# Kernel tuning notes

Hardware: AMD Instinct MI355X
Metric: run time of the kernel (lower is better)

Reference implementation:

```python
import jax, jax.numpy as jnp
import numpy as np

EPS = 1e-6  # matches nn.CosineSimilarity(eps=1e-6) and the log-denominator eps


def setup_inputs() -> dict:
    key = jax.random.key(0)
    k1, k2 = jax.random.split(key)
    bs, d = 8192, 128
    f = jax.random.normal(k1, (bs, d), dtype=jnp.float32)
    noise = jax.random.normal(k2, (bs, d), dtype=jnp.float32)
    return {"f": f, "noise": noise}


def reference(f, noise):
    bs = f.shape[0]
    cat = jnp.concatenate([noise, f], axis=0)  # [2bs, d]
    # torch CosineSimilarity: x.y / max(||x||*||y||, eps)
    nf = jnp.linalg.norm(f, axis=1)    # [bs]
    nc = jnp.linalg.norm(cat, axis=1)  # [2bs]
    sims = (f @ cat.T) / jnp.maximum(nf[:, None] * nc[None, :], EPS)  # [bs, 2bs]
    m = jnp.exp(sims)
    idx = jnp.arange(bs)
    pos = m[idx, idx]                 # f[i] vs noise[i]
    self_sim = m[idx, idx + bs]       # f[i] vs f[i], excluded from negatives
    neg_sum = m.sum(axis=1) - pos - self_sim
    loss = -jnp.log(pos / (neg_sum + EPS))
    return loss.mean()
```

## Files before the change

### kernel.cpp

```cpp
#include <hip/hip_runtime.h>
#include <hip/hip_bf16.h>
#include <math.h>

#define BS 8192
#define D 128
#define NROWS 16384
#define COLS_PER_BLOCK 512
#define NCHUNK (COLS_PER_BLOCK / 16)
#define NSPLIT (NROWS / COLS_PER_BLOCK)
#define NPART NSPLIT

typedef int i32x8 __attribute__((ext_vector_type(8)));
typedef float f32x4 __attribute__((ext_vector_type(4)));

#define LN2F 0.6931471805599453f
#define STORE_SCALE 19.217958569050494f
#define E8M0_M4 123

#if __has_builtin(__builtin_amdgcn_exp2f)
#define EXP2F(x) __builtin_amdgcn_exp2f(x)
#else
#define EXP2F(x) exp2f(x)
#endif


__global__ __launch_bounds__(256) void nrm_cvt(const float* __restrict__ f,
                                               const float* __restrict__ noise,
                                               char* __restrict__ catF) {
  const int lane = threadIdx.x & 63;
  const int wv = threadIdx.x >> 6;
  const int row = blockIdx.x * 4 + wv;
  const float* src = (row < BS) ? (noise + (size_t)row * D) : (f + (size_t)(row - BS) * D);
  float2 v = ((const float2*)src)[lane];
  float ss = v.x * v.x + v.y * v.y;
#pragma unroll
  for (int m = 1; m <= 32; m <<= 1) ss += __shfl_xor(ss, m, 64);
  const float s = STORE_SCALE / sqrtf(ss);
  const int packed = __builtin_amdgcn_cvt_pk_fp8_f32(v.x * s, v.y * s, 0, false);
  char* dst = catF + ((size_t)(row >> 4) << 11) + ((lane >> 4) << 9) +
              ((row & 15) << 5) + ((lane & 15) << 1);
  *(unsigned short*)dst = (unsigned short)(packed & 0xffff);
}

__global__ __launch_bounds__(256) void infonce_main(
    const char* __restrict__ catF,
    float* __restrict__ ws_neg, float* __restrict__ ws_pos) {
  const int tid = threadIdx.x;
  const int lane = tid & 63;
  const int w = tid >> 6;
  const int l15 = lane & 15, l4 = lane >> 4;
  const int nb = blockIdx.x, mb = blockIdx.y;
  const int growbase = mb * 128 + w * 32;
  const int col0 = nb * COLS_PER_BLOCK;
  const int lbase = l4 * 512 + l15 * 32;

  i32x8 a[2];
  {
    const char* ab = catF + ((size_t)((BS + growbase) >> 4) << 11) + lbase;
    a[0] = *(const i32x8*)(ab);
    a[1] = *(const i32x8*)(ab + 2048);
  }

  f32x4 rs[2];
  const f32x4 z = {0.f, 0.f, 0.f, 0.f};
  rs[0] = z;
  rs[1] = z;

  const char* bl = catF + ((size_t)(col0 >> 4) << 11) + lbase;

  i32x8 bb[2];
  bb[0] = *(const i32x8*)(bl);

#pragma unroll
  for (int ch = 0; ch < NCHUNK; ++ch) {
    const int cu = ch & 1;
    if (ch + 1 < NCHUNK)
      bb[cu ^ 1] = *(const i32x8*)(bl + (size_t)(ch + 1) * 2048);

    f32x4 acc[2];
#pragma unroll
    for (int rf = 0; rf < 2; rf++)
      acc[rf] = __builtin_amdgcn_mfma_scale_f32_16x16x128_f8f6f4(
          a[rf], bb[cu], z, 0 , 0 ,
          0, E8M0_M4, 0, E8M0_M4);

    const int c0 = col0 + ch * 16;
    const bool dPos = (c0 >= growbase) && (c0 < growbase + 32);
    const bool dSelf = (c0 - BS >= growbase) && (c0 - BS < growbase + 32);
    if (!dPos && !dSelf) {
#pragma unroll
      for (int rf = 0; rf < 2; rf++) {
        f32x4 e;
#pragma unroll
        for (int r = 0; r < 4; r++) e[r] = EXP2F(acc[rf][r]);
        rs[rf] += e;
      }
    } else {
#pragma unroll
      for (int rf = 0; rf < 2; rf++)
#pragma unroll
        for (int r = 0; r < 4; r++) {
          const int grow = growbase + rf * 16 + l4 * 4 + r;
          const int gcol = c0 + l15;
          const float v = acc[rf][r];
          const bool ex = dPos ? (gcol == grow) : (gcol == grow + BS);
          if (dPos && gcol == grow) ws_pos[grow] = v;
          rs[rf][r] += ex ? 0.f : EXP2F(v);
        }
    }
  }

  float rowsum[8];
#pragma unroll
  for (int rf = 0; rf < 2; rf++)
#pragma unroll
    for (int r = 0; r < 4; r++) {
      float v = rs[rf][r];
      v += __shfl_xor(v, 1, 64);
      v += __shfl_xor(v, 2, 64);
      v += __shfl_xor(v, 4, 64);
      v += __shfl_xor(v, 8, 64);
      rowsum[rf * 4 + r] = v;
    }
  if (l15 == 0) {
    float* dst = ws_neg + (size_t)nb * BS + growbase;
#pragma unroll
    for (int rf = 0; rf < 2; rf++)
#pragma unroll
      for (int r = 0; r < 4; r++) dst[rf * 16 + l4 * 4 + r] = rowsum[rf * 4 + r];
  }
}

__global__ __launch_bounds__(256) void finalize1(const float* __restrict__ ws_neg,
                                                 const float* __restrict__ ws_pos,
                                                 float* __restrict__ partial) {
  const int row = blockIdx.x * 256 + threadIdx.x;
  float neg = 0.f;
#pragma unroll
  for (int p = 0; p < NPART; p++) neg += ws_neg[(size_t)p * BS + row];
  float local = logf(neg + 1e-6f) - ws_pos[row] * LN2F;
#pragma unroll
  for (int m = 1; m <= 32; m <<= 1) local += __shfl_xor(local, m, 64);
  __shared__ float red[4];
  if ((threadIdx.x & 63) == 0) red[threadIdx.x >> 6] = local;
  __syncthreads();
  if (threadIdx.x == 0) partial[blockIdx.x] = red[0] + red[1] + red[2] + red[3];
}

__global__ void finalize2(const float* __restrict__ partial, float* __restrict__ out) {
  float v = ((int)threadIdx.x < 32) ? partial[threadIdx.x] : 0.f;
#pragma unroll
  for (int m = 1; m <= 32; m <<= 1) v += __shfl_xor(v, m, 64);
  if (threadIdx.x == 0) out[0] = v * (1.f / BS);
}

extern "C" void kernel_launch(void* const* d_in, const int* in_sizes, int n_in,
                              void* d_out, int out_size, void* d_ws, size_t ws_size,
                              hipStream_t stream) {
  const float* f = (const float*)d_in[0];
  const float* noise = (const float*)d_in[1];
  char* ws = (char*)d_ws;
  char* catF = ws;
  float* ws_pos = (float*)(ws + (size_t)NROWS * D);
  float* ws_neg = ws_pos + BS;
  float* partial = ws_neg + (size_t)NPART * BS;

  nrm_cvt<<<NROWS / 4, 256, 0, stream>>>(f, noise, catF);
  dim3 grid(NSPLIT, BS / 128);
  infonce_main<<<grid, 256, 0, stream>>>(catF, ws_neg, ws_pos);
  finalize1<<<BS / 256, 256, 0, stream>>>(ws_neg, ws_pos, partial);
  finalize2<<<1, 64, 0, stream>>>(partial, (float*)d_out);
}
```

Before: 41.42 us.

## Fuse finalize into main kernel via last-block atomic, deepen B prefetch

Drops the two finalize kernel launches by having the last block to finish (tracked by an atomic counter reset in the conversion kernel) perform the row reduction and log-mean in one block. Doubles the columns per block (1024, 16 splits) and switches to a 4-deep B-fragment ring with two chunks of MFMAs issued per phase before their epilogues. This removes launch overhead and halves partial-sum traffic. The trade-off is a serial single-block tail reduction over all 8192 rows and fewer, longer blocks.

```diff
diff --git a/kernel.cpp b/kernel.cpp
--- a/kernel.cpp
+++ b/kernel.cpp
@@ -5,10 +5,11 @@
 #define BS 8192
 #define D 128
 #define NROWS 16384
-#define COLS_PER_BLOCK 512
+#define NSPLIT 16
+#define COLS_PER_BLOCK 1024
 #define NCHUNK (COLS_PER_BLOCK / 16)
-#define NSPLIT (NROWS / COLS_PER_BLOCK)
 #define NPART NSPLIT
+#define NBLK (NSPLIT * (BS / 128))
 
 typedef int i32x8 __attribute__((ext_vector_type(8)));
 typedef float f32x4 __attribute__((ext_vector_type(4)));
@@ -26,7 +27,9 @@
 
 __global__ __launch_bounds__(256) void nrm_cvt(const float* __restrict__ f,
                                                const float* __restrict__ noise,
-                                               char* __restrict__ catF) {
+                                               char* __restrict__ catF,
+                                               unsigned int* __restrict__ cnt) {
+  if (blockIdx.x == 0 && threadIdx.x == 0) cnt[0] = 0;
   const int lane = threadIdx.x & 63;
   const int wv = threadIdx.x >> 6;
   const int row = blockIdx.x * 4 + wv;
@@ -44,7 +47,10 @@
 
 __global__ __launch_bounds__(256) void infonce_main(
     const char* __restrict__ catF,
-    float* __restrict__ ws_neg, float* __restrict__ ws_pos) {
+    float* __restrict__ ws_neg, float* __restrict__ ws_pos,
+    unsigned int* __restrict__ cnt, float* __restrict__ out) {
+  __shared__ int flag;
+  __shared__ float red[4];
   const int tid = threadIdx.x;
   const int lane = tid & 63;
   const int w = tid >> 6;
@@ -68,23 +74,13 @@
 
   const char* bl = catF + ((size_t)(col0 >> 4) << 11) + lbase;
 
-  i32x8 bb[2];
+  i32x8 bb[4];
   bb[0] = *(const i32x8*)(bl);
+  bb[1] = *(const i32x8*)(bl + 2048);
+  bb[2] = *(const i32x8*)(bl + 4096);
+  bb[3] = *(const i32x8*)(bl + 6144);
 
-#pragma unroll
-  for (int ch = 0; ch < NCHUNK; ++ch) {
-    const int cu = ch & 1;
-    if (ch + 1 < NCHUNK)
-      bb[cu ^ 1] = *(const i32x8*)(bl + (size_t)(ch + 1) * 2048);
-
-    f32x4 acc[2];
-#pragma unroll
-    for (int rf = 0; rf < 2; rf++)
-      acc[rf] = __builtin_amdgcn_mfma_scale_f32_16x16x128_f8f6f4(
-          a[rf], bb[cu], z, 0 , 0 ,
-          0, E8M0_M4, 0, E8M0_M4);
-
-    const int c0 = col0 + ch * 16;
+  auto epi = [&](const f32x4* acc, int c0) {
     const bool dPos = (c0 >= growbase) && (c0 < growbase + 32);
     const bool dSelf = (c0 - BS >= growbase) && (c0 - BS < growbase + 32);
     if (!dPos && !dSelf) {
@@ -108,6 +104,29 @@
           rs[rf][r] += ex ? 0.f : EXP2F(v);
         }
     }
+  };
+
+#pragma unroll
+  for (int ph = 0; ph < NCHUNK / 2; ++ph) {
+    const int c = 2 * ph;
+    const int s0 = c & 3;
+    const int s1 = s0 + 1;
+
+    f32x4 accA[2], accB[2];
+#pragma unroll
+    for (int rf = 0; rf < 2; rf++)
+      accA[rf] = __builtin_amdgcn_mfma_scale_f32_16x16x128_f8f6f4(
+          a[rf], bb[s0], z, 0, 0, 0, E8M0_M4, 0, E8M0_M4);
+#pragma unroll
+    for (int rf = 0; rf < 2; rf++)
+      accB[rf] = __builtin_amdgcn_mfma_scale_f32_16x16x128_f8f6f4(
+          a[rf], bb[s1], z, 0, 0, 0, E8M0_M4, 0, E8M0_M4);
+
+    if (c + 4 < NCHUNK) bb[s0] = *(const i32x8*)(bl + (size_t)(c + 4) * 2048);
+    if (c + 5 < NCHUNK) bb[s1] = *(const i32x8*)(bl + (size_t)(c + 5) * 2048);
+
+    epi(accA, col0 + c * 16);
+    epi(accB, col0 + c * 16 + 16);
   }
 
   float rowsum[8];
@@ -129,29 +148,28 @@
 #pragma unroll
       for (int r = 0; r < 4; r++) dst[rf * 16 + l4 * 4 + r] = rowsum[rf * 4 + r];
   }
-}
 
-__global__ __launch_bounds__(256) void finalize1(const float* __restrict__ ws_neg,
-                                                 const float* __restrict__ ws_pos,
-                                                 float* __restrict__ partial) {
-  const int row = blockIdx.x * 256 + threadIdx.x;
-  float neg = 0.f;
+  __syncthreads();
+  if (tid == 0) {
+    __threadfence();
+    flag = (atomicAdd(cnt, 1u) == (unsigned)(NBLK - 1));
+  }
+  __syncthreads();
+  if (!flag) return;
+  __threadfence();
+
+  float local = 0.f;
+  for (int row = tid; row < BS; row += 256) {
+    float neg = 0.f;
 #pragma unroll
-  for (int p = 0; p < NPART; p++) neg += ws_neg[(size_t)p * BS + row];
-  float local = logf(neg + 1e-6f) - ws_pos[row] * LN2F;
+    for (int p = 0; p < NPART; p++) neg += ws_neg[(size_t)p * BS + row];
+    local += logf(neg + 1e-6f) - ws_pos[row] * LN2F;
+  }
 #pragma unroll
   for (int m = 1; m <= 32; m <<= 1) local += __shfl_xor(local, m, 64);
-  __shared__ float red[4];
-  if ((threadIdx.x & 63) == 0) red[threadIdx.x >> 6] = local;
+  if (lane == 0) red[w] = local;
   __syncthreads();
-  if (threadIdx.x == 0) partial[blockIdx.x] = red[0] + red[1] + red[2] + red[3];
-}
-
-__global__ void finalize2(const float* __restrict__ partial, float* __restrict__ out) {
-  float v = ((int)threadIdx.x < 32) ? partial[threadIdx.x] : 0.f;
-#pragma unroll
-  for (int m = 1; m <= 32; m <<= 1) v += __shfl_xor(v, m, 64);
-  if (threadIdx.x == 0) out[0] = v * (1.f / BS);
+  if (tid == 0) out[0] = (red[0] + red[1] + red[2] + red[3]) * (1.f / BS);
 }
 
 extern "C" void kernel_launch(void* const* d_in, const int* in_sizes, int n_in,
@@ -163,11 +181,9 @@
   char* catF = ws;
   float* ws_pos = (float*)(ws + (size_t)NROWS * D);
   float* ws_neg = ws_pos + BS;
-  float* partial = ws_neg + (size_t)NPART * BS;
+  unsigned int* cnt = (unsigned int*)(ws_neg + (size_t)NPART * BS);
 
-  nrm_cvt<<<NROWS / 4, 256, 0, stream>>>(f, noise, catF);
+  nrm_cvt<<<NROWS / 4, 256, 0, stream>>>(f, noise, catF, cnt);
   dim3 grid(NSPLIT, BS / 128);
-  infonce_main<<<grid, 256, 0, stream>>>(catF, ws_neg, ws_pos);
-  finalize1<<<BS / 256, 256, 0, stream>>>(ws_neg, ws_pos, partial);
-  finalize2<<<1, 64, 0, stream>>>(partial, (float*)d_out);
+  infonce_main<<<grid, 256, 0, stream>>>(catF, ws_neg, ws_pos, cnt, (float*)d_out);
 }
```

Result: slower. 67.85 us (+63.8%).
